# Optimization experiments

Measured on AMD Instinct MI355X. Metric: run time of the kernel, lower is better.

Reference implementation:

```python
import jax, jax.numpy as jnp
import numpy as np

D = 1024
H = 16
DK = D // H
E = 8
DFF = 4 * D
TOPK = 2
EPS = 1e-5


def setup_inputs() -> dict:
    key = jax.random.key(0)
    ks = jax.random.split(key, 16)
    s_in = 1.0 / np.sqrt(D)
    s_ff = 1.0 / np.sqrt(DFF)
    return {
        "x": jax.random.normal(ks[0], (2, 2048, D), dtype=jnp.float32),
        "ln1_g": jnp.ones((D,), jnp.float32),
        "ln1_b": jnp.zeros((D,), jnp.float32),
        "w_qkv": jax.random.normal(ks[1], (D, 3 * D), jnp.float32) * s_in,
        "b_qkv": jnp.zeros((3 * D,), jnp.float32),
        "w_o": jax.random.normal(ks[2], (D, D), jnp.float32) * s_in,
        "b_o": jnp.zeros((D,), jnp.float32),
        "ln2_g": jnp.ones((D,), jnp.float32),
        "ln2_b": jnp.zeros((D,), jnp.float32),
        "gate_w": jax.random.normal(ks[3], (D, E), jnp.float32) * s_in,
        "gate_b": jnp.zeros((E,), jnp.float32),
        "W1": jax.random.normal(ks[4], (E, D, DFF), jnp.float32) * s_in,
        "b1": jnp.zeros((E, DFF), jnp.float32),
        "W2": jax.random.normal(ks[5], (E, DFF, D), jnp.float32) * s_ff,
        "b2": jnp.zeros((E, D), jnp.float32),
    }


def _layernorm(x, g, b):
    m = jnp.mean(x, axis=-1, keepdims=True)
    v = jnp.mean(jnp.square(x - m), axis=-1, keepdims=True)
    return (x - m) * jax.lax.rsqrt(v + EPS) * g + b


def reference(x, ln1_g, ln1_b, w_qkv, b_qkv, w_o, b_o, ln2_g, ln2_b,
              gate_w, gate_b, W1, b1, W2, b2):
    B, S, _ = x.shape
    # --- attention (pre-LN, residual) ---
    h = _layernorm(x, ln1_g, ln1_b)
    qkv = h @ w_qkv + b_qkv                      # [B,S,3D]
    q, k, v = jnp.split(qkv, 3, axis=-1)
    q = q.reshape(B, S, H, DK)
    k = k.reshape(B, S, H, DK)
    v = v.reshape(B, S, H, DK)
    scores = jnp.einsum('bqhd,bkhd->bhqk', q, k) / np.sqrt(DK)
    attn = jax.nn.softmax(scores, axis=-1)
    o = jnp.einsum('bhqk,bkhd->bqhd', attn, v).reshape(B, S, D)
    x = x + o @ w_o + b_o
    # --- MoE (pre-LN, residual) ---
    h = _layernorm(x, ln2_g, ln2_b).reshape(B * S, D)   # [T,D]
    logits = h @ gate_w + gate_b                        # [T,E]
    topv, topi = jax.lax.top_k(logits, TOPK)            # [T,K]
    gw = jax.nn.softmax(topv, axis=-1)                  # [T,K]
    # per-token per-expert combine weight (0 if expert not selected)
    ew = jnp.sum(jax.nn.one_hot(topi, E, dtype=h.dtype) * gw[..., None], axis=1)  # [T,E]
    hid = jax.nn.relu(jnp.einsum('td,edf->etf', h, W1) + b1[:, None, :])  # [E,T,DFF]
    out_e = jnp.einsum('etf,efd->etd', hid, W2) + b2[:, None, :]          # [E,T,D]
    moe = jnp.einsum('etd,te->td', out_e, ew)
    return x + moe.reshape(B, S, D)
```

## Files before the change

### kernel.cpp

```cpp
#include <hip/hip_runtime.h>

#define TT 4096
#define SS 2048
#define DD 1024
#define NH 16
#define NE 8
#define DFFC 4096

typedef _Float16 h8  __attribute__((ext_vector_type(8)));
typedef _Float16 h4v __attribute__((ext_vector_type(4)));
typedef float    f4  __attribute__((ext_vector_type(4)));

typedef __attribute__((address_space(3))) void lds_void;
typedef __attribute__((address_space(1))) const void gbl_void;

__device__ __forceinline__ f4 mfma16(h8 a, h8 b, f4 c){
  return __builtin_amdgcn_mfma_f32_16x16x32_f16(a, b, c, 0, 0, 0);
}
__device__ __forceinline__ void fsplit(float x, _Float16& hi, _Float16& lo){
  _Float16 h = (_Float16)x; hi = h; lo = (_Float16)(x - (float)h);
}
__device__ __forceinline__ void gll16(const void* g, void* l){
  __builtin_amdgcn_global_load_lds((gbl_void*)g, (lds_void*)l, 16, 0, 0);
}

template<int SPLIT>
__global__ __launch_bounds__(256) void conv_t(
    const float* __restrict__ in, _Float16* __restrict__ oh, _Float16* __restrict__ ol,
    int K, int N)
{
  __shared__ float tile[64][65];
  const int n0 = blockIdx.x*64, k0 = blockIdx.y*64;
  const int tid = threadIdx.x;
  const float* inp = in + (size_t)blockIdx.z*K*N;
  #pragma unroll
  for (int p=0;p<4;++p){
    int row = p*16 + (tid>>4), col4 = (tid&15)*4;
    *(f4*)&tile[row][col4] = *(const f4*)(inp + (size_t)(k0+row)*N + n0 + col4);
  }
  __syncthreads();
  const size_t ob = (size_t)blockIdx.z*K*N;
  #pragma unroll
  for (int p=0;p<2;++p){
    int n = p*32 + (tid>>3), k8 = (tid&7)*8;
    h8 vh, vl;
    #pragma unroll
    for (int j=0;j<8;++j){
      float v = tile[k8+j][n];
      if constexpr (SPLIT){ _Float16 hi,lo; fsplit(v,hi,lo); vh[j]=hi; vl[j]=lo; }
      else vh[j] = (_Float16)v;
    }
    size_t o = ob + (size_t)(n0+n)*K + k0 + k8;
    *(h8*)(oh + o) = vh;
    if constexpr (SPLIT) *(h8*)(ol + o) = vl;
  }
}

template<int MODE>
__global__ __launch_bounds__(256) void ln_kernel(
    const float* __restrict__ in, const float* __restrict__ g, const float* __restrict__ b,
    _Float16* __restrict__ outHi, _Float16* __restrict__ outLo)
{
  const int t = blockIdx.x, tid = threadIdx.x;
  f4 v = ((const f4*)(in + (size_t)t*DD))[tid];
  float s = v.x+v.y+v.z+v.w;
  float q = v.x*v.x+v.y*v.y+v.z*v.z+v.w*v.w;
  #pragma unroll
  for (int off=32; off; off>>=1){ s += __shfl_xor(s,off); q += __shfl_xor(q,off); }
  __shared__ float red[8];
  int wid = tid>>6, lane = tid&63;
  if (lane==0){ red[wid]=s; red[4+wid]=q; }
  __syncthreads();
  s = red[0]+red[1]+red[2]+red[3];
  q = red[4]+red[5]+red[6]+red[7];
  float mean = s * (1.0f/DD);
  float var  = q * (1.0f/DD) - mean*mean;
  float vv = var + 1e-5f;
  float r = rsqrtf(vv);
  r = r * (1.5f - 0.5f*vv*r*r);
  f4 gv = ((const f4*)g)[tid], bv = ((const f4*)b)[tid];
  #pragma unroll
  for (int j=0;j<4;++j){
    float y = (v[j]-mean)*r*gv[j] + bv[j];
    size_t o = (size_t)t*DD + tid*4 + j;
    if constexpr (MODE==0){ _Float16 hi,lo; fsplit(y,hi,lo); outHi[o]=hi; outLo[o]=lo; }
    else { outHi[o]=(_Float16)y; }
  }
}

template<int MODE>
__global__ __launch_bounds__(256,3) void gemm_split3(
    const _Float16* __restrict__ Ah, const _Float16* __restrict__ Al,
    const _Float16* __restrict__ Bh, const _Float16* __restrict__ Bl,
    const float* __restrict__ bias,
    _Float16* __restrict__ Chi, _Float16* __restrict__ Clo,
    float* __restrict__ Cf, const float* __restrict__ resid,
    int N, int K, int GM)
{
  __shared__ __align__(16) char smem[32768];
  const int tid = threadIdx.x, lane = tid&63, wid = tid>>6;
  const int l15 = lane&15, l4 = lane>>4;
  const int bid = blockIdx.x;
  const int c = bid & 7, rr = bid >> 3, mpx = GM >> 3;
  const int tm = (c*mpx + (rr % mpx))*128, tn = (rr / mpx)*128;

  const _Float16* sA[4]; const _Float16* sB[4];
  #pragma unroll
  for (int i=0;i<4;++i){
    int row = i*32 + (tid>>3);
    int s = (tid&7) ^ (row&7);
    int plane = s>>2, koff = (s&3)*8;
    sA[i] = (plane ? Al : Ah) + (size_t)(tm+row)*K + koff;
    sB[i] = (plane ? Bl : Bh) + (size_t)(tn+row)*K + koff;
  }
  int offAh[4], offAl[4], offBh[4], offBl[4];
  #pragma unroll
  for (int m=0;m<4;++m){
    int rowA = (wid>>1)*64 + m*16 + l15;
    offAh[m] = rowA*64 + ((l4 ^ (rowA&7))<<3);
    offAl[m] = rowA*64 + (((4|l4) ^ (rowA&7))<<3);
    int rowB = (wid&1)*64 + m*16 + l15;
    offBh[m] = rowB*64 + ((l4 ^ (rowB&7))<<3);
    offBl[m] = rowB*64 + (((4|l4) ^ (rowB&7))<<3);
  }
  f4 acc[4][4] = {};
  const _Float16* As = (const _Float16*)(smem);
  const _Float16* Bs = (const _Float16*)(smem + 16384);
  for (int k0=0; k0<K; k0+=32){
    #pragma unroll
    for (int i=0;i<4;++i){
      int L = i*4096 + tid*16;
      gll16(sA[i]+k0, smem + L);
      gll16(sB[i]+k0, smem + 16384 + L);
    }
    __syncthreads();
    h8 ah[4], al[4], bh4[4], bl4[4];
    #pragma unroll
    for (int m=0;m<4;++m){ ah[m] = *(const h8*)&As[offAh[m]]; al[m] = *(const h8*)&As[offAl[m]]; }
    #pragma unroll
    for (int n=0;n<4;++n){ bh4[n] = *(const h8*)&Bs[offBh[n]]; bl4[n] = *(const h8*)&Bs[offBl[n]]; }
    #pragma unroll
    for (int n=0;n<4;++n)
      #pragma unroll
      for (int m=0;m<4;++m){
        acc[m][n] = mfma16(ah[m], bh4[n], acc[m][n]);
        acc[m][n] = mfma16(ah[m], bl4[n], acc[m][n]);
        acc[m][n] = mfma16(al[m], bh4[n], acc[m][n]);
      }
    __syncthreads();
  }
  const int wm = (wid>>1)*64, wn = (wid&1)*64;
  #pragma unroll
  for (int n=0;n<4;++n){
    int col = tn + wn + n*16 + l15;
    float bv = bias[col];
    #pragma unroll
    for (int m=0;m<4;++m)
      #pragma unroll
      for (int r=0;r<4;++r){
        int rowg = tm + wm + m*16 + l4*4 + r;
        float vv = acc[m][n][r] + bv;
        size_t co = (size_t)rowg*N + col;
        if constexpr (MODE==0){ _Float16 hi,lo; fsplit(vv,hi,lo); Chi[co]=hi; Clo[co]=lo; }
        else { Cf[co] = vv + resid[co]; }
      }
  }
}

__global__ __launch_bounds__(256) void vt_kernel(
    const _Float16* __restrict__ qkvH, const _Float16* __restrict__ qkvL,
    _Float16* __restrict__ vtH, _Float16* __restrict__ vtL)
{
  __shared__ _Float16 TH[64*72], TL[64*72];
  const int tid = threadIdx.x;
  const int tt = blockIdx.x*64;
  const int bh = blockIdx.y;
  const int b = bh>>4, h = bh&15;
  const size_t t0 = (size_t)b*SS;
  #pragma unroll
  for (int p=0;p<2;++p){
    int t = p*32 + (tid>>3), d0 = (tid&7)*8;
    size_t g = (t0 + tt + t)*(size_t)3072 + 2048 + h*64 + d0;
    h8 vh = *(const h8*)(qkvH+g), vl = *(const h8*)(qkvL+g);
    int cp = ((t>>3) ^ (tid&7)) & 7;
    int base = cp*8 + (t&7);
    #pragma unroll
    for (int j=0;j<8;++j){ TH[(d0+j)*72 + base] = vh[j]; TL[(d0+j)*72 + base] = vl[j]; }
  }
  __syncthreads();
  int d = tid>>2, seg = tid&3;
  size_t ob = ((size_t)bh*64 + d)*2048 + tt;
  #pragma unroll
  for (int jj=0;jj<2;++jj){
    int cch = jj*4 + seg, cp = (cch ^ (d>>3)) & 7;
    h8 vh = *(const h8*)&TH[d*72 + cp*8];
    h8 vl = *(const h8*)&TL[d*72 + cp*8];
    *(h8*)(vtH + ob + cch*8) = vh;
    *(h8*)(vtL + ob + cch*8) = vl;
  }
}

__global__ __launch_bounds__(256,3) void attn_kernel(
    const _Float16* __restrict__ qkvH, const _Float16* __restrict__ qkvL,
    const _Float16* __restrict__ vtH, const _Float16* __restrict__ vtL,
    _Float16* __restrict__ oH, _Float16* __restrict__ oL)
{
  __shared__ __align__(16) _Float16 KsH[64*64], KsL[64*64], VsH[64*64], VsL[64*64];
  __shared__ __align__(16) _Float16 Plds[10240];
  const int tid = threadIdx.x, lane = tid & 63, wid = tid >> 6;
  const int l15 = lane & 15, l4 = lane >> 4;
  const int qt = blockIdx.x, bh = blockIdx.y;
  const int b = bh >> 4, h = bh & 15;
  const size_t t0 = (size_t)b * SS;
  const int qbase = qt*128 + wid*32;

  const int srow = tid>>3;
  const int ss = (tid&7) ^ (srow&7);
  const _Float16* kH = qkvH + (t0 + srow)*(size_t)3072 + 1024 + h*64 + ss*8;
  const _Float16* kL = qkvL + (t0 + srow)*(size_t)3072 + 1024 + h*64 + ss*8;
  const _Float16* vH = vtH + ((size_t)bh*64 + srow)*2048 + ss*8;
  const _Float16* vL = vtL + ((size_t)bh*64 + srow)*2048 + ss*8;
  const int ldsL0 = tid*16;

  int offF[4][2];
  #pragma unroll
  for (int n=0;n<4;++n)
    #pragma unroll
    for (int ks=0;ks<2;++ks){
      int row = n*16 + l15;
      offF[n][ks] = row*64 + (((ks*4 + l4) ^ (row&7))<<3);
    }
  int pq[2], prb[2];
  #pragma unroll
  for (int m=0;m<2;++m){
    int q = m*16 + l15;
    pq[m]  = wid*5120 + q*80;
    prb[m] = pq[m] + l4*16;
  }

  h8 qh[2][2], ql[2][2];
  #pragma unroll
  for (int m=0;m<2;++m)
    #pragma unroll
    for (int ks=0;ks<2;++ks){
      size_t go = (t0 + qbase + m*16 + l15)*(size_t)3072 + h*64 + ks*32 + l4*8;
      qh[m][ks] = *(const h8*)(qkvH + go);
      ql[m][ks] = *(const h8*)(qkvL + go);
    }

  f4 oacc[2][4] = {};
  float psum[2] = {0.f, 0.f};

  for (int kv=0; kv<SS; kv+=64){
    #pragma unroll
    for (int cc=0; cc<2; ++cc){
      size_t kgo = (size_t)(kv + cc*32)*3072;
      size_t vgo = (size_t)kv + (size_t)cc*32*2048;
      int L = cc*4096 + ldsL0;
      gll16(kH + kgo, (char*)KsH + L);
      gll16(kL + kgo, (char*)KsL + L);
      gll16(vH + vgo, (char*)VsH + L);
      gll16(vL + vgo, (char*)VsL + L);
    }
    __syncthreads();

    #pragma unroll
    for (int half=0; half<2; ++half){
      f4 s[2][2] = {};
      __builtin_amdgcn_s_setprio(1);
      #pragma unroll
      for (int n2=0;n2<2;++n2){
        int nn = half*2 + n2;
        #pragma unroll
        for (int ks=0;ks<2;++ks){
          h8 kh = *(const h8*)&KsH[offF[nn][ks]];
          h8 kl = *(const h8*)&KsL[offF[nn][ks]];
          s[0][n2] = mfma16(kh, qh[0][ks], s[0][n2]);
          s[0][n2] = mfma16(kl, qh[0][ks], s[0][n2]);
          s[0][n2] = mfma16(kh, ql[0][ks], s[0][n2]);
          s[1][n2] = mfma16(kh, qh[1][ks], s[1][n2]);
          s[1][n2] = mfma16(kl, qh[1][ks], s[1][n2]);
          s[1][n2] = mfma16(kh, ql[1][ks], s[1][n2]);
        }
      }
      __builtin_amdgcn_s_setprio(0);
      #pragma unroll
      for (int m=0;m<2;++m){
        #pragma unroll
        for (int n2=0;n2<2;++n2){
          f4 sv = s[m][n2];
          float p0 = __expf(fmaf(sv.x, 0.125f, -8.0f));
          float p1 = __expf(fmaf(sv.y, 0.125f, -8.0f));
          float p2 = __expf(fmaf(sv.z, 0.125f, -8.0f));
          float p3 = __expf(fmaf(sv.w, 0.125f, -8.0f));
          psum[m] += (p0+p1)+(p2+p3);
          h4v hv, lv; _Float16 hh, ll;
          fsplit(p0,hh,ll); hv[0]=hh; lv[0]=ll;
          fsplit(p1,hh,ll); hv[1]=hh; lv[1]=ll;
          fsplit(p2,hh,ll); hv[2]=hh; lv[2]=ll;
          fsplit(p3,hh,ll); hv[3]=hh; lv[3]=ll;
          int wb = pq[m] + n2*32 + l4*8;
          *(h4v*)((char*)Plds + wb) = hv;
          *(h4v*)((char*)Plds + 2560 + wb) = lv;
        }
      }
      __builtin_amdgcn_s_setprio(1);
      h8 paH0 = *(const h8*)((char*)Plds + prb[0]);
      h8 paL0 = *(const h8*)((char*)Plds + 2560 + prb[0]);
      h8 paH1 = *(const h8*)((char*)Plds + prb[1]);
      h8 paL1 = *(const h8*)((char*)Plds + 2560 + prb[1]);
      #pragma unroll
      for (int nd=0;nd<4;++nd){
        h8 vh = *(const h8*)&VsH[offF[nd][half]];
        h8 vl = *(const h8*)&VsL[offF[nd][half]];
        oacc[0][nd] = mfma16(paH0, vh, oacc[0][nd]);
        oacc[0][nd] = mfma16(paH0, vl, oacc[0][nd]);
        oacc[0][nd] = mfma16(paL0, vh, oacc[0][nd]);
        oacc[1][nd] = mfma16(paH1, vh, oacc[1][nd]);
        oacc[1][nd] = mfma16(paH1, vl, oacc[1][nd]);
        oacc[1][nd] = mfma16(paL1, vh, oacc[1][nd]);
      }
      __builtin_amdgcn_s_setprio(0);
    }
    __syncthreads();
  }

  #pragma unroll
  for (int m=0;m<2;++m){
    float ls = psum[m];
    ls += __shfl_xor(ls, 16);
    ls += __shfl_xor(ls, 32);
    #pragma unroll
    for (int r=0;r<4;++r){
      int srcl = l4*4 + r;
      float lq = __uint_as_float(
          (unsigned)__builtin_amdgcn_ds_bpermute(srcl*4, (int)__float_as_uint(ls)));
      float linv = 1.0f / lq;
      #pragma unroll
      for (int nd=0;nd<4;++nd){
        float vv = oacc[m][nd][r] * linv;
        size_t go = (t0 + qbase + m*16 + l4*4 + r)*(size_t)DD + h*64 + nd*16 + l15;
        _Float16 hi, lo; fsplit(vv, hi, lo);
        oH[go] = hi; oL[go] = lo;
      }
    }
  }
}

__global__ __launch_bounds__(256) void gate_kernel(
    const float* __restrict__ x1, const float* __restrict__ g, const float* __restrict__ bb,
    const float* __restrict__ gw, const float* __restrict__ gb,
    int* __restrict__ topi, float* __restrict__ topw, int* __restrict__ cnt)
{
  const int t = blockIdx.x*4 + (threadIdx.x>>6), lane = threadIdx.x & 63;
  f4 xv[4];
  float s=0.f, q=0.f;
  #pragma unroll
  for (int i=0;i<4;++i){
    xv[i] = ((const f4*)(x1 + (size_t)t*DD))[lane + i*64];
    #pragma unroll
    for (int j=0;j<4;++j){ s += xv[i][j]; q += xv[i][j]*xv[i][j]; }
  }
  #pragma unroll
  for (int off=32; off; off>>=1){ s += __shfl_xor(s,off); q += __shfl_xor(q,off); }
  float mean = s*(1.f/DD), var = q*(1.f/DD)-mean*mean, vv = var+1e-5f;
  float r = rsqrtf(vv); r = r*(1.5f-0.5f*vv*r*r);
  float acc[8] = {0,0,0,0,0,0,0,0};
  #pragma unroll
  for (int i=0;i<4;++i){
    f4 gv = ((const f4*)g)[lane+i*64], bv = ((const f4*)bb)[lane+i*64];
    #pragma unroll
    for (int j=0;j<4;++j){
      int d = (lane+i*64)*4 + j;
      float hv = (xv[i][j]-mean)*r*gv[j] + bv[j];
      const f4* gp = (const f4*)(gw + (size_t)d*8);
      f4 g0 = gp[0], g1 = gp[1];
      acc[0]+=hv*g0.x; acc[1]+=hv*g0.y; acc[2]+=hv*g0.z; acc[3]+=hv*g0.w;
      acc[4]+=hv*g1.x; acc[5]+=hv*g1.y; acc[6]+=hv*g1.z; acc[7]+=hv*g1.w;
    }
  }
  #pragma unroll
  for (int e=0;e<8;++e)
    #pragma unroll
    for (int off=32;off;off>>=1) acc[e]+=__shfl_xor(acc[e],off);
  if (lane==0){
    float lg[8];
    #pragma unroll
    for (int e=0;e<8;++e) lg[e]=acc[e]+gb[e];
    int i0=0; float v0=lg[0];
    #pragma unroll
    for (int e=1;e<8;++e) if (lg[e]>v0){ v0=lg[e]; i0=e; }
    int i1=-1; float v1=-1e30f;
    #pragma unroll
    for (int e=0;e<8;++e) if (e!=i0 && lg[e]>v1){ v1=lg[e]; i1=e; }
    float w0 = 1.f/(1.f+__expf(v1-v0));
    topi[2*t]=i0; topi[2*t+1]=i1;
    topw[2*t]=w0; topw[2*t+1]=1.f-w0;
    atomicAdd(&cnt[i0],1); atomicAdd(&cnt[i1],1);
  }
}

__global__ void scan_kernel(const int* __restrict__ cnt, int* __restrict__ offs,
                            int* __restrict__ cursor, int* __restrict__ pref1,
                            int* __restrict__ pref2){
  if (threadIdx.x==0){
    int s=0, t1=0, t2=0;
    for (int e=0;e<8;++e){
      offs[e]=s; s+=cnt[e];
      int mt = (cnt[e]+127)>>7;
      pref1[e]=t1; t1 += mt*(DFFC/128);
      pref2[e]=t2; t2 += mt*(DD/128)*2;
    }
    offs[8]=s; pref1[8]=t1; pref2[8]=t2;
  }
  if (threadIdx.x<8) cursor[threadIdx.x]=0;
}

__global__ __launch_bounds__(256) void scatter_kernel(
    const int* __restrict__ topi, const int* __restrict__ offs, int* __restrict__ cursor,
    int* __restrict__ tokl, int* __restrict__ posof)
{
  int t = blockIdx.x*256 + threadIdx.x;
  #pragma unroll
  for (int k=0;k<2;++k){
    int e = topi[2*t+k];
    int p = atomicAdd(&cursor[e],1);
    int idx = offs[e]+p;
    tokl[idx]=t; posof[2*t+k]=idx;
  }
}

template<int GATHER, int KH>
__global__ __launch_bounds__(256,4) void gemm_ffn(
    const _Float16* __restrict__ A, const _Float16* __restrict__ Bw,
    const float* __restrict__ bias, _Float16* __restrict__ C0, _Float16* __restrict__ C1,
    const int* __restrict__ tok, const int* __restrict__ offs,
    const int* __restrict__ pref, int N, int K)
{
  __shared__ __align__(16) char smem[32768];
  const int tid = threadIdx.x, lane = tid&63, wid = tid>>6;
  const int l15 = lane&15, l4 = lane>>4;
  const int wm = (wid>>1)*64, wn = (wid&1)*64;
  const int tot = pref[8];
  const int nt = N>>7;
  const int KSEG = K/KH;

  int offA[4][2], offB[4][2];
  #pragma unroll
  for (int m=0;m<4;++m)
    #pragma unroll
    for (int ks=0;ks<2;++ks){
      int rowA = wm + m*16 + l15;
      offA[m][ks] = rowA*64 + (((ks*4+l4) ^ (rowA&7))<<3);
      int rowB = wn + m*16 + l15;
      offB[m][ks] = rowB*64 + (((ks*4+l4) ^ (rowB&7))<<3);
    }

  const int cpx = gridDim.x >> 3;
  const int bswz = (blockIdx.x & 7)*cpx + (blockIdx.x >> 3);
  for (int idx = bswz; idx < tot; idx += gridDim.x){
    int e = 0;
    #pragma unroll
    for (int k=1;k<8;++k) if (pref[k] <= idx) e = k;
    const int off = offs[e], Me = offs[e+1]-off;
    const int mt = (Me+127)>>7;
    int local = idx - pref[e];
    int kh = 0;
    if constexpr (KH==2){ int per = mt*nt; kh = (local >= per); local -= kh*per; }
    const int ni = local / mt, mi = local - ni*mt;
    const int tm = mi*128, tn = ni*128;
    const int kb = kh*KSEG;
    const _Float16* Bp = Bw + (size_t)e*N*K + (size_t)tn*K;
    const float* biasp = bias + (size_t)e*N;

    const _Float16* sA[4]; const _Float16* sB[4];
    #pragma unroll
    for (int i=0;i<4;++i){
      int row = i*32 + (tid>>3);
      int s = (tid&7) ^ (row&7);
      int lr = min(tm+row, Me-1);
      size_t ar = GATHER ? (size_t)tok[off+lr] : (size_t)(off+lr);
      sA[i] = A + ar*K + s*8 + kb;
      sB[i] = Bp + (size_t)row*K + s*8 + kb;
    }
    f4 acc[4][4] = {};
    const _Float16* As = (const _Float16*)(smem);
    const _Float16* Bs = (const _Float16*)(smem + 16384);
    for (int k0=0; k0<KSEG; k0+=64){
      #pragma unroll
      for (int i=0;i<4;++i){
        int L = i*4096 + tid*16;
        gll16(sA[i]+k0, smem + L);
        gll16(sB[i]+k0, smem + 16384 + L);
      }
      __syncthreads();
      #pragma unroll
      for (int ks=0;ks<2;++ks){
        h8 av[4], bv[4];
        #pragma unroll
        for (int m=0;m<4;++m) av[m] = *(const h8*)&As[offA[m][ks]];
        #pragma unroll
        for (int n=0;n<4;++n) bv[n] = *(const h8*)&Bs[offB[n][ks]];
        #pragma unroll
        for (int n=0;n<4;++n)
          #pragma unroll
          for (int m=0;m<4;++m)
            acc[m][n] = mfma16(av[m], bv[n], acc[m][n]);
      }
      __syncthreads();
    }
    _Float16* Cp = (KH==2 && kh==1) ? C1 : C0;
    _Float16* Cs = (_Float16*)smem;
    float bvv[4];
    #pragma unroll
    for (int n=0;n<4;++n) bvv[n] = (KH==2 && kh==1) ? 0.f : biasp[tn + wn + n*16 + l15];
    #pragma unroll
    for (int p=0;p<2;++p){
      if ((wid&1)==p){
        #pragma unroll
        for (int n=0;n<4;++n)
          #pragma unroll
          for (int m=0;m<4;++m)
            #pragma unroll
            for (int r=0;r<4;++r){
              int row = wm + m*16 + l4*4 + r;
              float vv = acc[m][n][r] + bvv[n];
              if constexpr (GATHER) vv = fmaxf(vv, 0.f);
              Cs[row*72 + n*16 + l15] = (_Float16)vv;
            }
      }
      __syncthreads();
      int row = tid>>1, seg = tid&1;
      if (tm+row < Me){
        size_t gb = (size_t)(off+tm+row)*N + tn + p*64 + seg*32;
        #pragma unroll
        for (int j=0;j<4;++j)
          *(h8*)(Cp + gb + j*8) = *(const h8*)&Cs[row*72 + seg*32 + j*8];
      }
      __syncthreads();
    }
  }
}

__global__ __launch_bounds__(256) void combine_kernel(
    const float* __restrict__ x1, const _Float16* __restrict__ moe0,
    const _Float16* __restrict__ moe1,
    const float* __restrict__ topw, const int* __restrict__ posof, float* __restrict__ out)
{
  int t = blockIdx.x, tid = threadIdx.x;
  size_t o = (size_t)t*DD + tid*4;
  f4 xv = *(const f4*)(x1+o);
  int p0=posof[2*t], p1=posof[2*t+1];
  float w0=topw[2*t], w1=topw[2*t+1];
  h4v a0 = *(const h4v*)(moe0 + (size_t)p0*DD + tid*4);
  h4v b0 = *(const h4v*)(moe1 + (size_t)p0*DD + tid*4);
  h4v a1 = *(const h4v*)(moe0 + (size_t)p1*DD + tid*4);
  h4v b1 = *(const h4v*)(moe1 + (size_t)p1*DD + tid*4);
  f4 r;
  #pragma unroll
  for (int j=0;j<4;++j)
    r[j] = xv[j] + w0*((float)a0[j]+(float)b0[j]) + w1*((float)a1[j]+(float)b1[j]);
  *(f4*)(out+o) = r;
}

extern "C" void kernel_launch(void* const* d_in, const int* in_sizes, int n_in,
                              void* d_out, int out_size, void* d_ws, size_t ws_size,
                              hipStream_t stream)
{
  (void)in_sizes; (void)n_in; (void)out_size; (void)ws_size;
  const float* x     = (const float*)d_in[0];
  const float* ln1g  = (const float*)d_in[1];
  const float* ln1b  = (const float*)d_in[2];
  const float* wqkv  = (const float*)d_in[3];
  const float* bqkv  = (const float*)d_in[4];
  const float* wo    = (const float*)d_in[5];
  const float* bo    = (const float*)d_in[6];
  const float* ln2g  = (const float*)d_in[7];
  const float* ln2b  = (const float*)d_in[8];
  const float* gatew = (const float*)d_in[9];
  const float* gateb = (const float*)d_in[10];
  const float* W1    = (const float*)d_in[11];
  const float* b1    = (const float*)d_in[12];
  const float* W2    = (const float*)d_in[13];
  const float* b2    = (const float*)d_in[14];
  float* out = (float*)d_out;

  char* w = (char*)d_ws;
  _Float16* W1T    = (_Float16*)(w);
  _Float16* W2T    = (_Float16*)(w + 67108864);
  _Float16* wqT_H  = (_Float16*)(w + 134217728);
  _Float16* wqT_L  = (_Float16*)(w + 140509184);
  _Float16* woT_H  = (_Float16*)(w + 146800640);
  _Float16* woT_L  = (_Float16*)(w + 148897792);
  _Float16* moe1   = (_Float16*)(w + 134217728);
  char* rb = w + 150994944;
  _Float16* h1H  = (_Float16*)(rb);
  _Float16* h1L  = (_Float16*)(rb + 8388608);
  _Float16* vtH  = (_Float16*)(rb);
  _Float16* vtL  = (_Float16*)(rb + 8388608);
  _Float16* qkvH = (_Float16*)(rb + 16777216);
  _Float16* qkvL = (_Float16*)(rb + 41943040);
  _Float16* hid  = (_Float16*)(rb);
  char* rm = w + 218103808;
  _Float16* oH   = (_Float16*)(rm);
  _Float16* oL   = (_Float16*)(rm + 8388608);
  _Float16* moe0 = (_Float16*)(rm);
  float* x1     = (float*)(w + 234881024);
  _Float16* h2h = (_Float16*)(w + 251658240);
  char* sm = w + 260046848;
  float* topw  = (float*)(sm);
  int*   topi  = (int*)(sm + 32768);
  int*   posof = (int*)(sm + 65536);
  int*   tokl  = (int*)(sm + 98304);
  int*   cnt   = (int*)(sm + 131072);
  int*   offs  = (int*)(sm + 131072 + 64);
  int*   cursor= (int*)(sm + 131072 + 128);
  int*   pref1 = (int*)(sm + 131072 + 192);
  int*   pref2 = (int*)(sm + 131072 + 256);

  conv_t<1><<<dim3(48, 16, 1), 256, 0, stream>>>(wqkv, wqT_H, wqT_L, 1024, 3072);
  conv_t<1><<<dim3(16, 16, 1), 256, 0, stream>>>(wo,   woT_H, woT_L, 1024, 1024);
  conv_t<0><<<dim3(64, 16, 8), 256, 0, stream>>>(W1, W1T, nullptr, 1024, 4096);
  conv_t<0><<<dim3(16, 64, 8), 256, 0, stream>>>(W2, W2T, nullptr, 4096, 1024);

  ln_kernel<0><<<TT, 256, 0, stream>>>(x, ln1g, ln1b, h1H, h1L);
  gemm_split3<0><<<768, 256, 0, stream>>>(
      h1H, h1L, wqT_H, wqT_L, bqkv, qkvH, qkvL, nullptr, nullptr, 3072, 1024, 32);
  vt_kernel<<<dim3(32, 32), 256, 0, stream>>>(qkvH, qkvL, vtH, vtL);
  attn_kernel<<<dim3(SS/128, 2*NH), 256, 0, stream>>>(qkvH, qkvL, vtH, vtL, oH, oL);
  gemm_split3<1><<<256, 256, 0, stream>>>(
      oH, oL, woT_H, woT_L, bo, nullptr, nullptr, x1, x, 1024, 1024, 32);
  ln_kernel<1><<<TT, 256, 0, stream>>>(x1, ln2g, ln2b, h2h, nullptr);
  hipMemsetAsync(cnt, 0, 8*sizeof(int), stream);
  gate_kernel<<<TT/4, 256, 0, stream>>>(x1, ln2g, ln2b, gatew, gateb, topi, topw, cnt);
  scan_kernel<<<1, 32, 0, stream>>>(cnt, offs, cursor, pref1, pref2);
  scatter_kernel<<<TT/256, 256, 0, stream>>>(topi, offs, cursor, tokl, posof);
  gemm_ffn<1,1><<<1024, 256, 0, stream>>>(
      h2h, W1T, b1, hid, hid, tokl, offs, pref1, DFFC, 1024);
  gemm_ffn<0,2><<<1024, 256, 0, stream>>>(
      hid, W2T, b2, moe0, moe1, tokl, offs, pref2, DD, DFFC);
  combine_kernel<<<TT, 256, 0, stream>>>(x1, moe0, moe1, topw, posof, out);
}
```

Baseline: 725.3 us.

## Prefetch next K-slice into LDS while computing in QKV and FFN GEMMs

The split-precision QKV GEMM now loads the next k-slice into LDS right after reading the current fragments into registers, so global loads overlap the MFMA work. The FFN GEMM drops its 64-wide K step for a 32-wide one and double-buffers LDS across two 16KB halves with a new swizzle, issuing loads for the next step before computing the current one. This aims to hide global-to-LDS latency. In exchange it adds more loop iterations and barriers per K, and correctness relies on the async LDS loads finishing at each single barrier.

Result: slower. 744.9 us (+2.7%).

```diff
diff --git a/kernel.cpp b/kernel.cpp
--- a/kernel.cpp
+++ b/kernel.cpp
@@ -123,22 +123,31 @@
     offBh[m] = rowB*64 + ((l4 ^ (rowB&7))<<3);
     offBl[m] = rowB*64 + (((4|l4) ^ (rowB&7))<<3);
   }
+  #pragma unroll
+  for (int i=0;i<4;++i){
+    int L = i*4096 + tid*16;
+    gll16(sA[i], smem + L);
+    gll16(sB[i], smem + 16384 + L);
+  }
+  __syncthreads();
   f4 acc[4][4] = {};
   const _Float16* As = (const _Float16*)(smem);
   const _Float16* Bs = (const _Float16*)(smem + 16384);
   for (int k0=0; k0<K; k0+=32){
-    #pragma unroll
-    for (int i=0;i<4;++i){
-      int L = i*4096 + tid*16;
-      gll16(sA[i]+k0, smem + L);
-      gll16(sB[i]+k0, smem + 16384 + L);
-    }
+    h8 ah[4], al[4], bh4[4], bl4[4];
+    #pragma unroll
+    for (int m=0;m<4;++m){ ah[m] = *(const h8*)&As[offAh[m]]; al[m] = *(const h8*)&As[offAl[m]]; }
+    #pragma unroll
+    for (int n=0;n<4;++n){ bh4[n] = *(const h8*)&Bs[offBh[n]]; bl4[n] = *(const h8*)&Bs[offBl[n]]; }
     __syncthreads();
-    h8 ah[4], al[4], bh4[4], bl4[4];
-    #pragma unroll
-    for (int m=0;m<4;++m){ ah[m] = *(const h8*)&As[offAh[m]]; al[m] = *(const h8*)&As[offAl[m]]; }
-    #pragma unroll
-    for (int n=0;n<4;++n){ bh4[n] = *(const h8*)&Bs[offBh[n]]; bl4[n] = *(const h8*)&Bs[offBl[n]]; }
+    if (k0+32 < K){
+      #pragma unroll
+      for (int i=0;i<4;++i){
+        int L = i*4096 + tid*16;
+        gll16(sA[i]+k0+32, smem + L);
+        gll16(sB[i]+k0+32, smem + 16384 + L);
+      }
+    }
     #pragma unroll
     for (int n=0;n<4;++n)
       #pragma unroll
@@ -445,16 +454,14 @@
   const int nt = N>>7;
   const int KSEG = K/KH;
 
-  int offA[4][2], offB[4][2];
-  #pragma unroll
-  for (int m=0;m<4;++m)
-    #pragma unroll
-    for (int ks=0;ks<2;++ks){
-      int rowA = wm + m*16 + l15;
-      offA[m][ks] = rowA*64 + (((ks*4+l4) ^ (rowA&7))<<3);
-      int rowB = wn + m*16 + l15;
-      offB[m][ks] = rowB*64 + (((ks*4+l4) ^ (rowB&7))<<3);
-    }
+  int offA[4], offB[4];
+  #pragma unroll
+  for (int m=0;m<4;++m){
+    int rowA = wm + m*16 + l15;
+    offA[m] = rowA*32 + ((l4 ^ (rowA&3))<<3);
+    int rowB = wn + m*16 + l15;
+    offB[m] = rowB*32 + ((l4 ^ (rowB&3))<<3);
+  }
 
   const int cpx = gridDim.x >> 3;
   const int bswz = (blockIdx.x & 7)*cpx + (blockIdx.x >> 3);
@@ -473,41 +480,49 @@
     const _Float16* Bp = Bw + (size_t)e*N*K + (size_t)tn*K;
     const float* biasp = bias + (size_t)e*N;
 
-    const _Float16* sA[4]; const _Float16* sB[4];
-    #pragma unroll
-    for (int i=0;i<4;++i){
-      int row = i*32 + (tid>>3);
-      int s = (tid&7) ^ (row&7);
+    const _Float16* sA[2]; const _Float16* sB[2];
+    #pragma unroll
+    for (int i=0;i<2;++i){
+      int row = i*64 + (tid>>2);
+      int s = (tid&3) ^ (row&3);
       int lr = min(tm+row, Me-1);
       size_t ar = GATHER ? (size_t)tok[off+lr] : (size_t)(off+lr);
       sA[i] = A + ar*K + s*8 + kb;
       sB[i] = Bp + (size_t)row*K + s*8 + kb;
     }
+    #pragma unroll
+    for (int i=0;i<2;++i){
+      int L = i*4096 + tid*16;
+      gll16(sA[i], smem + L);
+      gll16(sB[i], smem + 8192 + L);
+    }
+    __syncthreads();
     f4 acc[4][4] = {};
-    const _Float16* As = (const _Float16*)(smem);
-    const _Float16* Bs = (const _Float16*)(smem + 16384);
-    for (int k0=0; k0<KSEG; k0+=64){
-      #pragma unroll
-      for (int i=0;i<4;++i){
-        int L = i*4096 + tid*16;
-        gll16(sA[i]+k0, smem + L);
-        gll16(sB[i]+k0, smem + 16384 + L);
-      }
+    int cur = 0;
+    for (int k0=0; k0<KSEG; k0+=32){
+      if (k0+32 < KSEG){
+        int nb = (cur^1)*16384;
+        #pragma unroll
+        for (int i=0;i<2;++i){
+          int L = i*4096 + tid*16;
+          gll16(sA[i]+k0+32, smem + nb + L);
+          gll16(sB[i]+k0+32, smem + nb + 8192 + L);
+        }
+      }
+      const _Float16* As = (const _Float16*)(smem + cur*16384);
+      const _Float16* Bs = (const _Float16*)(smem + cur*16384 + 8192);
+      h8 av[4], bv[4];
+      #pragma unroll
+      for (int m=0;m<4;++m) av[m] = *(const h8*)&As[offA[m]];
+      #pragma unroll
+      for (int n=0;n<4;++n) bv[n] = *(const h8*)&Bs[offB[n]];
+      #pragma unroll
+      for (int n=0;n<4;++n)
+        #pragma unroll
+        for (int m=0;m<4;++m)
+          acc[m][n] = mfma16(av[m], bv[n], acc[m][n]);
       __syncthreads();
-      #pragma unroll
-      for (int ks=0;ks<2;++ks){
-        h8 av[4], bv[4];
-        #pragma unroll
-        for (int m=0;m<4;++m) av[m] = *(const h8*)&As[offA[m][ks]];
-        #pragma unroll
-        for (int n=0;n<4;++n) bv[n] = *(const h8*)&Bs[offB[n][ks]];
-        #pragma unroll
-        for (int n=0;n<4;++n)
-          #pragma unroll
-          for (int m=0;m<4;++m)
-            acc[m][n] = mfma16(av[m], bv[n], acc[m][n]);
-      }
-      __syncthreads();
+      cur ^= 1;
     }
     _Float16* Cp = (KH==2 && kh==1) ? C1 : C0;
     _Float16* Cs = (_Float16*)smem;
```

## Prefetch next K-tile into LDS during MFMA compute in GEMM loops

Applied to the files above, without the earlier changes.

In two GEMM kernels (the split-precision QKV/out GEMM and the grouped MoE expert GEMM), the main loop now reads the current tile from LDS into registers, syncs, then issues global_load_lds for the next K-tile before running the MFMAs. The first tile is preloaded before the loop. This lets global-to-LDS traffic overlap with matrix math inside a single LDS buffer, replacing the load-wait-compute serialization. It costs more live registers for the fragments, which may reduce occupancy.

After: 1.562 ms. +115.4%, slower.

```diff
diff --git a/kernel.cpp b/kernel.cpp
--- a/kernel.cpp
+++ b/kernel.cpp
@@ -123,22 +123,31 @@
     offBh[m] = rowB*64 + ((l4 ^ (rowB&7))<<3);
     offBl[m] = rowB*64 + (((4|l4) ^ (rowB&7))<<3);
   }
+  #pragma unroll
+  for (int i=0;i<4;++i){
+    int L = i*4096 + tid*16;
+    gll16(sA[i], smem + L);
+    gll16(sB[i], smem + 16384 + L);
+  }
+  __syncthreads();
   f4 acc[4][4] = {};
   const _Float16* As = (const _Float16*)(smem);
   const _Float16* Bs = (const _Float16*)(smem + 16384);
   for (int k0=0; k0<K; k0+=32){
-    #pragma unroll
-    for (int i=0;i<4;++i){
-      int L = i*4096 + tid*16;
-      gll16(sA[i]+k0, smem + L);
-      gll16(sB[i]+k0, smem + 16384 + L);
-    }
+    h8 ah[4], al[4], bh4[4], bl4[4];
+    #pragma unroll
+    for (int m=0;m<4;++m){ ah[m] = *(const h8*)&As[offAh[m]]; al[m] = *(const h8*)&As[offAl[m]]; }
+    #pragma unroll
+    for (int n=0;n<4;++n){ bh4[n] = *(const h8*)&Bs[offBh[n]]; bl4[n] = *(const h8*)&Bs[offBl[n]]; }
     __syncthreads();
-    h8 ah[4], al[4], bh4[4], bl4[4];
-    #pragma unroll
-    for (int m=0;m<4;++m){ ah[m] = *(const h8*)&As[offAh[m]]; al[m] = *(const h8*)&As[offAl[m]]; }
-    #pragma unroll
-    for (int n=0;n<4;++n){ bh4[n] = *(const h8*)&Bs[offBh[n]]; bl4[n] = *(const h8*)&Bs[offBl[n]]; }
+    if (k0+32 < K){
+      #pragma unroll
+      for (int i=0;i<4;++i){
+        int L = i*4096 + tid*16;
+        gll16(sA[i]+k0+32, smem + L);
+        gll16(sB[i]+k0+32, smem + 16384 + L);
+      }
+    }
     #pragma unroll
     for (int n=0;n<4;++n)
       #pragma unroll
@@ -483,30 +492,41 @@
       sA[i] = A + ar*K + s*8 + kb;
       sB[i] = Bp + (size_t)row*K + s*8 + kb;
     }
+    #pragma unroll
+    for (int i=0;i<4;++i){
+      int L = i*4096 + tid*16;
+      gll16(sA[i], smem + L);
+      gll16(sB[i], smem + 16384 + L);
+    }
+    __syncthreads();
     f4 acc[4][4] = {};
     const _Float16* As = (const _Float16*)(smem);
     const _Float16* Bs = (const _Float16*)(smem + 16384);
     for (int k0=0; k0<KSEG; k0+=64){
-      #pragma unroll
-      for (int i=0;i<4;++i){
-        int L = i*4096 + tid*16;
-        gll16(sA[i]+k0, smem + L);
-        gll16(sB[i]+k0, smem + 16384 + L);
+      h8 av[4][2], bv[4][2];
+      #pragma unroll
+      for (int ks=0;ks<2;++ks){
+        #pragma unroll
+        for (int m=0;m<4;++m) av[m][ks] = *(const h8*)&As[offA[m][ks]];
+        #pragma unroll
+        for (int n=0;n<4;++n) bv[n][ks] = *(const h8*)&Bs[offB[n][ks]];
       }
       __syncthreads();
-      #pragma unroll
-      for (int ks=0;ks<2;++ks){
-        h8 av[4], bv[4];
-        #pragma unroll
-        for (int m=0;m<4;++m) av[m] = *(const h8*)&As[offA[m][ks]];
-        #pragma unroll
-        for (int n=0;n<4;++n) bv[n] = *(const h8*)&Bs[offB[n][ks]];
+      if (k0+64 < KSEG){
+        #pragma unroll
+        for (int i=0;i<4;++i){
+          int L = i*4096 + tid*16;
+          gll16(sA[i]+k0+64, smem + L);
+          gll16(sB[i]+k0+64, smem + 16384 + L);
+        }
+      }
+      #pragma unroll
+      for (int ks=0;ks<2;++ks)
         #pragma unroll
         for (int n=0;n<4;++n)
           #pragma unroll
           for (int m=0;m<4;++m)
-            acc[m][n] = mfma16(av[m], bv[n], acc[m][n]);
-      }
+            acc[m][n] = mfma16(av[m][ks], bv[n][ks], acc[m][n]);
       __syncthreads();
     }
     _Float16* Cp = (KH==2 && kh==1) ? C1 : C0;
```
